# Kernel optimization log

Hardware: AMD Instinct MI355X
Metric: run time of the kernel (lower is better)

Reference implementation:

```python
import jax, jax.numpy as jnp
import numpy as np

N_NODES = 50000
N_EDGES = 600000
F_IN = 128
HID = 128
N_CLASSES = 10
N_GRAPHS = 64


def _glorot(key, shape):
    fan_in, fan_out = shape[1], shape[0]
    lim = float(np.sqrt(6.0 / (fan_in + fan_out)))
    return jax.random.uniform(key, shape, jnp.float32, -lim, lim)


def setup_inputs() -> dict:
    key = jax.random.key(0)
    ks = jax.random.split(key, 16)
    x = jax.random.normal(ks[0], (N_NODES, F_IN), jnp.float32)
    edge_index = jax.random.randint(ks[1], (2, N_EDGES), 0, N_NODES, jnp.int64)
    batch = jnp.sort(jax.random.randint(ks[2], (N_NODES,), 0, N_GRAPHS, jnp.int64))
    # GraphConv params: lin_rel (with bias) applied to aggregated neighbor sum,
    # lin_root (no bias) applied to the node's own features.
    params = dict(
        W1_rel=_glorot(ks[3], (HID, F_IN)), b1_rel=jnp.zeros((HID,), jnp.float32),
        W1_root=_glorot(ks[4], (HID, F_IN)),
        W2_rel=_glorot(ks[5], (HID, HID)), b2_rel=jnp.zeros((HID,), jnp.float32),
        W2_root=_glorot(ks[6], (HID, HID)),
        W3_rel=_glorot(ks[7], (HID, HID)), b3_rel=jnp.zeros((HID,), jnp.float32),
        W3_root=_glorot(ks[8], (HID, HID)),
        W_lin=_glorot(ks[9], (N_CLASSES, HID)), b_lin=jnp.zeros((N_CLASSES,), jnp.float32),
    )
    return {"x": x, "edge_index": edge_index, "batch": batch, **params}


def _graph_conv(x, src, dst, W_rel, b_rel, W_root):
    # gather source features, scatter-add into targets, then linear (sum aggr
    # commutes with the linear, matching PyG GraphConv which applies lin_rel
    # after aggregation)
    agg = jax.ops.segment_sum(x[src], dst, num_segments=N_NODES)  # [N, F]
    return agg @ W_rel.T + b_rel + x @ W_root.T


def _mean_pool(x, batch):
    sums = jax.ops.segment_sum(x, batch, num_segments=N_GRAPHS)  # [G, H]
    cnts = jax.ops.segment_sum(jnp.ones((x.shape[0],), x.dtype), batch,
                               num_segments=N_GRAPHS)
    return sums / jnp.maximum(cnts, 1.0)[:, None]


def reference(x, edge_index, batch,
              W1_rel, b1_rel, W1_root,
              W2_rel, b2_rel, W2_root,
              W3_rel, b3_rel, W3_root,
              W_lin, b_lin):
    src, dst = edge_index[0], edge_index[1]
    h = jax.nn.relu(_graph_conv(x, src, dst, W1_rel, b1_rel, W1_root))
    h = jax.nn.relu(_graph_conv(h, src, dst, W2_rel, b2_rel, W2_root))
    h = _graph_conv(h, src, dst, W3_rel, b3_rel, W3_root)
    g = _mean_pool(h, batch)  # [G, H]
    # dropout is identity in eval mode (training=False)
    return g @ W_lin.T + b_lin  # [G, num_classes]
```

## Files before the change

### kernel.cpp

```cpp
#include <hip/hip_runtime.h>
#include <hip/hip_bf16.h>

#define N_NODES   50000
#define N_EDGES   600000
#define F         128
#define N_GRAPHS  64
#define N_CLASSES 10
#define NPAD      50048
#define NB_SCAN   196
#define XCVT_BLOCKS 6250

typedef __attribute__((ext_vector_type(8))) short bf16x8;
typedef __attribute__((ext_vector_type(4))) float f32x4;

static __device__ __forceinline__ unsigned short f2bf(float f) {
    __hip_bfloat16 h = __float2bfloat16(f);
    return *reinterpret_cast<unsigned short*>(&h);
}
static __device__ __forceinline__ float bf2f(unsigned short u) {
    return __uint_as_float(((unsigned)u) << 16);
}

__global__ __launch_bounds__(256) void hist_kernel(
    const int* __restrict__ dst, int* __restrict__ deg)
{
    int e = blockIdx.x * 256 + threadIdx.x;
    if (e >= N_EDGES) return;
    atomicAdd(&deg[dst[e]], 1);
}

__global__ __launch_bounds__(256) void scanA_kernel(
    const int* __restrict__ deg, int* __restrict__ locEx, int* __restrict__ blockSum)
{
    __shared__ int sh[256];
    int t = threadIdx.x;
    int idx = blockIdx.x * 256 + t;
    int v = (idx < N_NODES) ? deg[idx] : 0;
    sh[t] = v;
    __syncthreads();
#pragma unroll
    for (int d = 1; d < 256; d <<= 1) {
        int u = (t >= d) ? sh[t - d] : 0;
        __syncthreads();
        sh[t] += u;
        __syncthreads();
    }
    if (idx < N_NODES) locEx[idx] = sh[t] - v;
    if (t == 255) blockSum[blockIdx.x] = sh[255];
}

__global__ __launch_bounds__(256) void scanBC_kernel(
    const int* __restrict__ locEx, const int* __restrict__ blockSum,
    int* __restrict__ off)
{
    __shared__ int sh[256];
    int t = threadIdx.x;
    int v = (t < NB_SCAN) ? blockSum[t] : 0;
    sh[t] = v;
    __syncthreads();
#pragma unroll
    for (int d = 1; d < 256; d <<= 1) {
        int u = (t >= d) ? sh[t - d] : 0;
        __syncthreads();
        sh[t] += u;
        __syncthreads();
    }
    int myVal  = blockSum[blockIdx.x];
    int base   = sh[blockIdx.x] - myVal;
    int idx = blockIdx.x * 256 + t;
    if (idx < N_NODES) off[idx] = locEx[idx] + base;
    if (blockIdx.x == 0 && t == 0) off[N_NODES] = sh[NB_SCAN - 1];
}

__global__ __launch_bounds__(256) void fill_kernel(
    const int* __restrict__ src, const int* __restrict__ dst,
    const int* __restrict__ off, int* __restrict__ cursor,
    int* __restrict__ csr_src)
{
    int e = blockIdx.x * 256 + threadIdx.x;
    if (e >= N_EDGES) return;
    int d = dst[e];
    int slot = atomicAdd(&cursor[d], 1);
    csr_src[off[d] + slot] = src[e];
}

__global__ __launch_bounds__(256) void cvt_all_kernel(
    const float* __restrict__ x,
    const float* __restrict__ W0, const float* __restrict__ W1,
    const float* __restrict__ W2, const float* __restrict__ W3,
    const float* __restrict__ W4, const float* __restrict__ W5,
    unsigned short* __restrict__ Xb, unsigned short* __restrict__ Wb)
{
    int b = blockIdx.x;
    if (b < XCVT_BLOCKS) {
        int i = b * 256 + threadIdx.x;
        float4 v = reinterpret_cast<const float4*>(x)[i];
        ushort4 o;
        o.x = f2bf(v.x); o.y = f2bf(v.y); o.z = f2bf(v.z); o.w = f2bf(v.w);
        reinterpret_cast<ushort4*>(Xb)[i] = o;
    } else {
        const int PER = (F * F / 4) / 256;
        int bb  = b - XCVT_BLOCKS;
        int mat = bb / PER;
        int i   = (bb % PER) * 256 + threadIdx.x;
        const float* W = (mat == 0) ? W0 : (mat == 1) ? W1 : (mat == 2) ? W2
                       : (mat == 3) ? W3 : (mat == 4) ? W4 : W5;
        float4 v = reinterpret_cast<const float4*>(W)[i];
        ushort4 o;
        o.x = f2bf(v.x); o.y = f2bf(v.y); o.z = f2bf(v.z); o.w = f2bf(v.w);
        reinterpret_cast<ushort4*>(Wb + (size_t)mat * F * F)[i] = o;
    }
}

template <int RELU>
__global__ __launch_bounds__(256) void conv_fused(
    const unsigned short* __restrict__ Xb,
    const int* __restrict__ off, const int* __restrict__ csr_src,
    const unsigned short* __restrict__ Wrel, const unsigned short* __restrict__ Wroot,
    const float* __restrict__ brel, unsigned short* __restrict__ H)
{
    __shared__ char AsRaw[64 * 256];
    const int t = threadIdx.x;
    const int mBase = blockIdx.x * 64;

    {
        const int r = t >> 2;
        const int q = t & 3;
        int row = mBase + r;
        float acc[32];
#pragma unroll
        for (int i = 0; i < 32; ++i) acc[i] = 0.f;
        if (row < N_NODES) {
            int s0 = off[row], s1 = off[row + 1];
            for (int j = s0; j < s1; ++j) {
                int s = csr_src[j];
                const bf16x8* base = reinterpret_cast<const bf16x8*>(
                    Xb + (size_t)s * F + q * 32);
#pragma unroll
                for (int c = 0; c < 4; ++c) {
                    bf16x8 v = base[c];
#pragma unroll
                    for (int e = 0; e < 8; ++e) acc[c * 8 + e] += bf2f((unsigned short)v[e]);
                }
            }
        }
#pragma unroll
        for (int c = 0; c < 4; ++c) {
            bf16x8 o;
#pragma unroll
            for (int e = 0; e < 8; ++e) o[e] = (short)f2bf(acc[c * 8 + e]);
            int bytecol = (q * 64 + c * 16) ^ ((r & 7) << 4);
            *reinterpret_cast<bf16x8*>(AsRaw + r * 256 + bytecol) = o;
        }
    }
    __syncthreads();

    const int wave = t >> 6;
    const int lane = t & 63;
    const int wm = wave >> 1, wn = wave & 1;
    const int m0l = wm * 32;
    const int n0  = wn * 64;
    const int lrow = lane & 15;
    const int lk8  = (lane >> 4) << 3;

    f32x4 acc[2][4];
#pragma unroll
    for (int mi = 0; mi < 2; ++mi)
#pragma unroll
        for (int ni = 0; ni < 4; ++ni)
            acc[mi][ni] = (f32x4){0.f, 0.f, 0.f, 0.f};

#pragma unroll
    for (int p = 0; p < 2; ++p) {
        const unsigned short* W = p ? Wroot : Wrel;
#pragma unroll
        for (int ks = 0; ks < 4; ++ks) {
            int k0 = ks * 32 + lk8;
            bf16x8 a[2], b[4];
#pragma unroll
            for (int mi = 0; mi < 2; ++mi) {
                int rl = m0l + mi * 16 + lrow;
                if (p == 0) {
                    int bytecol = (k0 * 2) ^ ((rl & 7) << 4);
                    a[mi] = *reinterpret_cast<const bf16x8*>(AsRaw + rl * 256 + bytecol);
                } else {
                    a[mi] = *reinterpret_cast<const bf16x8*>(
                        Xb + (size_t)(mBase + rl) * F + k0);
                }
            }
#pragma unroll
            for (int ni = 0; ni < 4; ++ni)
                b[ni] = *reinterpret_cast<const bf16x8*>(
                    W + (size_t)(n0 + ni * 16 + lrow) * F + k0);
#pragma unroll
            for (int mi = 0; mi < 2; ++mi)
#pragma unroll
                for (int ni = 0; ni < 4; ++ni)
                    acc[mi][ni] = __builtin_amdgcn_mfma_f32_16x16x32_bf16(
                        a[mi], b[ni], acc[mi][ni], 0, 0, 0);
        }
    }

    const int r0 = (lane >> 4) << 2;
#pragma unroll
    for (int ni = 0; ni < 4; ++ni) {
        int col = n0 + ni * 16 + lrow;
        float bb = brel[col];
#pragma unroll
        for (int mi = 0; mi < 2; ++mi) {
#pragma unroll
            for (int r = 0; r < 4; ++r) {
                int row = mBase + m0l + mi * 16 + r0 + r;
                if (row < N_NODES) {
                    float v = acc[mi][ni][r] + bb;
                    if (RELU) v = fmaxf(v, 0.f);
                    H[(size_t)row * F + col] = f2bf(v);
                }
            }
        }
    }
}

__global__ __launch_bounds__(256) void pool_kernel(
    const unsigned short* __restrict__ H, const int* __restrict__ batch,
    float* __restrict__ G)
{
    int g = blockIdx.x;
    int lo = 0, hi = N_NODES;
    while (lo < hi) { int m = (lo + hi) >> 1; if (batch[m] < g) lo = m + 1; else hi = m; }
    int start = lo;
    hi = N_NODES;
    while (lo < hi) { int m = (lo + hi) >> 1; if (batch[m] < g + 1) lo = m + 1; else hi = m; }
    int end = lo;

    int l8 = (threadIdx.x & 15) << 3;
    int rg = threadIdx.x >> 4;
    float acc[8] = {0.f, 0.f, 0.f, 0.f, 0.f, 0.f, 0.f, 0.f};
    for (int i = start + rg; i < end; i += 16) {
        bf16x8 v = *reinterpret_cast<const bf16x8*>(H + (size_t)i * F + l8);
#pragma unroll
        for (int r = 0; r < 8; ++r) acc[r] += bf2f((unsigned short)v[r]);
    }
    __shared__ float sh[16][F];
#pragma unroll
    for (int r = 0; r < 8; ++r) sh[rg][l8 + r] = acc[r];
    __syncthreads();
    if (threadIdx.x < F) {
        int f = threadIdx.x;
        float s = 0.f;
#pragma unroll
        for (int k = 0; k < 16; ++k) s += sh[k][f];
        float cnt = (float)(end - start);
        G[g * F + f] = s / fmaxf(cnt, 1.f);
    }
}

__global__ __launch_bounds__(640) void head_kernel(
    const float* __restrict__ G, const float* __restrict__ Wl,
    const float* __restrict__ bl, float* __restrict__ out)
{
    int t = threadIdx.x;
    int g = t / N_CLASSES;
    int c = t % N_CLASSES;
    float s = bl[c];
#pragma unroll 8
    for (int k = 0; k < F; ++k) s += G[g * F + k] * Wl[c * F + k];
    out[t] = s;
}

extern "C" void kernel_launch(void* const* d_in, const int* in_sizes, int n_in,
                              void* d_out, int out_size, void* d_ws, size_t ws_size,
                              hipStream_t stream)
{
    const float* x     = (const float*)d_in[0];
    const int*   edge  = (const int*)d_in[1];
    const int*   src   = edge;
    const int*   dst   = edge + N_EDGES;
    const int*   batch = (const int*)d_in[2];
    const float* W1r = (const float*)d_in[3];
    const float* b1  = (const float*)d_in[4];
    const float* W1o = (const float*)d_in[5];
    const float* W2r = (const float*)d_in[6];
    const float* b2  = (const float*)d_in[7];
    const float* W2o = (const float*)d_in[8];
    const float* W3r = (const float*)d_in[9];
    const float* b3  = (const float*)d_in[10];
    const float* W3o = (const float*)d_in[11];
    const float* Wl  = (const float*)d_in[12];
    const float* bl  = (const float*)d_in[13];
    float* out = (float*)d_out;

    char* ws = (char*)d_ws;
    const size_t fb = (size_t)NPAD * F * sizeof(unsigned short);
    unsigned short* Xb  = (unsigned short*)ws;
    unsigned short* H1b = (unsigned short*)(ws + fb);
    unsigned short* H2b = (unsigned short*)(ws + 2 * fb);
    char* p = ws + 3 * fb;
    unsigned short* Wb = (unsigned short*)p;
    p += (size_t)6 * F * F * sizeof(unsigned short);
    float* G = (float*)p;                p += (size_t)N_GRAPHS * F * sizeof(float);
    int* deg     = (int*)p;              p += (size_t)N_NODES * sizeof(int);
    int* cursor  = (int*)p;              p += (size_t)N_NODES * sizeof(int);
    int* off     = (int*)p;              p += (size_t)(N_NODES + 1) * sizeof(int);
    int* locEx   = (int*)p;              p += (size_t)N_NODES * sizeof(int);
    int* blockSum= (int*)p;              p += (size_t)256 * sizeof(int);
    int* csr_src = (int*)p;

    const int edgeBlocks = (N_EDGES + 255) / 256;
    const int convBlocks = NPAD / 64;
    const int cvtBlocks  = XCVT_BLOCKS + 6 * (F * F / 4) / 256;

    cvt_all_kernel<<<cvtBlocks, 256, 0, stream>>>(x, W1r, W1o, W2r, W2o, W3r, W3o, Xb, Wb);

    hipMemsetAsync(deg, 0, (size_t)2 * N_NODES * sizeof(int), stream);
    hist_kernel<<<edgeBlocks, 256, 0, stream>>>(dst, deg);
    scanA_kernel<<<NB_SCAN, 256, 0, stream>>>(deg, locEx, blockSum);
    scanBC_kernel<<<NB_SCAN, 256, 0, stream>>>(locEx, blockSum, off);
    fill_kernel<<<edgeBlocks, 256, 0, stream>>>(src, dst, off, cursor, csr_src);

    conv_fused<1><<<convBlocks, 256, 0, stream>>>(Xb,  off, csr_src, Wb + 0 * F * F, Wb + 1 * F * F, b1, H1b);
    conv_fused<1><<<convBlocks, 256, 0, stream>>>(H1b, off, csr_src, Wb + 2 * F * F, Wb + 3 * F * F, b2, H2b);
    conv_fused<0><<<convBlocks, 256, 0, stream>>>(H2b, off, csr_src, Wb + 4 * F * F, Wb + 5 * F * F, b3, H1b);

    pool_kernel<<<N_GRAPHS, 256, 0, stream>>>(H1b, batch, G);
    head_kernel<<<1, 640, 0, stream>>>(G, Wl, bl, out);
}
```

Baseline: 253.2 us.

## Halve conv tile rows, spread gather over 8 lanes per node, prefetch neighbor

Each conv block now handles 32 nodes instead of 64. Each node's neighbor aggregation is split across 8 threads of 16 features instead of 4 threads of 32. The gather loop software-prefetches the next neighbor's row before accumulating the current one. The aim is more gather parallelism and more blocks in flight to hide the latency of irregular memory accesses, at the cost of loading the weight tiles twice as often per node and doing half the MFMA work per wave.

Result: slower. 290.3 us (+14.7%).

```diff
diff --git a/kernel.cpp b/kernel.cpp
--- a/kernel.cpp
+++ b/kernel.cpp
@@ -9,6 +9,7 @@
 #define NPAD      50048
 #define NB_SCAN   196
 #define XCVT_BLOCKS 6250
+#define BM        32
 
 typedef __attribute__((ext_vector_type(8))) short bf16x8;
 typedef __attribute__((ext_vector_type(4))) float f32x4;
@@ -119,56 +120,66 @@
     const unsigned short* __restrict__ Wrel, const unsigned short* __restrict__ Wroot,
     const float* __restrict__ brel, unsigned short* __restrict__ H)
 {
-    __shared__ char AsRaw[64 * 256];
+    __shared__ char AsRaw[BM * 256];
     const int t = threadIdx.x;
-    const int mBase = blockIdx.x * 64;
+    const int mBase = blockIdx.x * BM;
 
     {
-        const int r = t >> 2;
-        const int q = t & 3;
+        const int r = t >> 3;
+        const int q = t & 7;
         int row = mBase + r;
-        float acc[32];
-#pragma unroll
-        for (int i = 0; i < 32; ++i) acc[i] = 0.f;
+        float acc[16];
+#pragma unroll
+        for (int i = 0; i < 16; ++i) acc[i] = 0.f;
         if (row < N_NODES) {
             int s0 = off[row], s1 = off[row + 1];
-            for (int j = s0; j < s1; ++j) {
-                int s = csr_src[j];
-                const bf16x8* base = reinterpret_cast<const bf16x8*>(
-                    Xb + (size_t)s * F + q * 32);
-#pragma unroll
-                for (int c = 0; c < 4; ++c) {
-                    bf16x8 v = base[c];
-#pragma unroll
-                    for (int e = 0; e < 8; ++e) acc[c * 8 + e] += bf2f((unsigned short)v[e]);
+            const unsigned short* Xq = Xb + (size_t)q * 16;
+            if (s0 < s1) {
+                int s = csr_src[s0];
+                bf16x8 v0 = *reinterpret_cast<const bf16x8*>(Xq + (size_t)s * F);
+                bf16x8 v1 = *reinterpret_cast<const bf16x8*>(Xq + (size_t)s * F + 8);
+                for (int j = s0 + 1; j < s1; ++j) {
+                    int sn = csr_src[j];
+                    bf16x8 u0 = *reinterpret_cast<const bf16x8*>(Xq + (size_t)sn * F);
+                    bf16x8 u1 = *reinterpret_cast<const bf16x8*>(Xq + (size_t)sn * F + 8);
+#pragma unroll
+                    for (int e = 0; e < 8; ++e) {
+                        acc[e]     += bf2f((unsigned short)v0[e]);
+                        acc[8 + e] += bf2f((unsigned short)v1[e]);
+                    }
+                    v0 = u0; v1 = u1;
+                }
+#pragma unroll
+                for (int e = 0; e < 8; ++e) {
+                    acc[e]     += bf2f((unsigned short)v0[e]);
+                    acc[8 + e] += bf2f((unsigned short)v1[e]);
                 }
             }
         }
-#pragma unroll
-        for (int c = 0; c < 4; ++c) {
-            bf16x8 o;
-#pragma unroll
-            for (int e = 0; e < 8; ++e) o[e] = (short)f2bf(acc[c * 8 + e]);
-            int bytecol = (q * 64 + c * 16) ^ ((r & 7) << 4);
-            *reinterpret_cast<bf16x8*>(AsRaw + r * 256 + bytecol) = o;
+        bf16x8 o0, o1;
+#pragma unroll
+        for (int e = 0; e < 8; ++e) {
+            o0[e] = (short)f2bf(acc[e]);
+            o1[e] = (short)f2bf(acc[8 + e]);
         }
+        int sw = (r & 7) << 4;
+        *reinterpret_cast<bf16x8*>(AsRaw + r * 256 + ((q * 32)      ^ sw)) = o0;
+        *reinterpret_cast<bf16x8*>(AsRaw + r * 256 + ((q * 32 + 16) ^ sw)) = o1;
     }
     __syncthreads();
 
     const int wave = t >> 6;
     const int lane = t & 63;
     const int wm = wave >> 1, wn = wave & 1;
-    const int m0l = wm * 32;
+    const int m0l = wm * 16;
     const int n0  = wn * 64;
     const int lrow = lane & 15;
     const int lk8  = (lane >> 4) << 3;
-
-    f32x4 acc[2][4];
-#pragma unroll
-    for (int mi = 0; mi < 2; ++mi)
-#pragma unroll
-        for (int ni = 0; ni < 4; ++ni)
-            acc[mi][ni] = (f32x4){0.f, 0.f, 0.f, 0.f};
+    const int arow = m0l + lrow;
+
+    f32x4 acc2[4];
+#pragma unroll
+    for (int ni = 0; ni < 4; ++ni) acc2[ni] = (f32x4){0.f, 0.f, 0.f, 0.f};
 
 #pragma unroll
     for (int p = 0; p < 2; ++p) {
@@ -176,28 +187,22 @@
 #pragma unroll
         for (int ks = 0; ks < 4; ++ks) {
             int k0 = ks * 32 + lk8;
-            bf16x8 a[2], b[4];
-#pragma unroll
-            for (int mi = 0; mi < 2; ++mi) {
-                int rl = m0l + mi * 16 + lrow;
-                if (p == 0) {
-                    int bytecol = (k0 * 2) ^ ((rl & 7) << 4);
-                    a[mi] = *reinterpret_cast<const bf16x8*>(AsRaw + rl * 256 + bytecol);
-                } else {
-                    a[mi] = *reinterpret_cast<const bf16x8*>(
-                        Xb + (size_t)(mBase + rl) * F + k0);
-                }
+            bf16x8 a, b[4];
+            if (p == 0) {
+                int bytecol = (k0 * 2) ^ ((arow & 7) << 4);
+                a = *reinterpret_cast<const bf16x8*>(AsRaw + arow * 256 + bytecol);
+            } else {
+                a = *reinterpret_cast<const bf16x8*>(
+                    Xb + (size_t)(mBase + arow) * F + k0);
             }
 #pragma unroll
             for (int ni = 0; ni < 4; ++ni)
                 b[ni] = *reinterpret_cast<const bf16x8*>(
                     W + (size_t)(n0 + ni * 16 + lrow) * F + k0);
 #pragma unroll
-            for (int mi = 0; mi < 2; ++mi)
-#pragma unroll
-                for (int ni = 0; ni < 4; ++ni)
-                    acc[mi][ni] = __builtin_amdgcn_mfma_f32_16x16x32_bf16(
-                        a[mi], b[ni], acc[mi][ni], 0, 0, 0);
+            for (int ni = 0; ni < 4; ++ni)
+                acc2[ni] = __builtin_amdgcn_mfma_f32_16x16x32_bf16(
+                    a, b[ni], acc2[ni], 0, 0, 0);
         }
     }
 
@@ -207,15 +212,12 @@
         int col = n0 + ni * 16 + lrow;
         float bb = brel[col];
 #pragma unroll
-        for (int mi = 0; mi < 2; ++mi) {
-#pragma unroll
-            for (int r = 0; r < 4; ++r) {
-                int row = mBase + m0l + mi * 16 + r0 + r;
-                if (row < N_NODES) {
-                    float v = acc[mi][ni][r] + bb;
-                    if (RELU) v = fmaxf(v, 0.f);
-                    H[(size_t)row * F + col] = f2bf(v);
-                }
+        for (int r = 0; r < 4; ++r) {
+            int row = mBase + m0l + r0 + r;
+            if (row < N_NODES) {
+                float v = acc2[ni][r] + bb;
+                if (RELU) v = fmaxf(v, 0.f);
+                H[(size_t)row * F + col] = f2bf(v);
             }
         }
     }
@@ -307,7 +309,7 @@
     int* csr_src = (int*)p;
 
     const int edgeBlocks = (N_EDGES + 255) / 256;
-    const int convBlocks = NPAD / 64;
+    const int convBlocks = NPAD / BM;
     const int cvtBlocks  = XCVT_BLOCKS + 6 * (F * F / 4) / 256;
 
     cvt_all_kernel<<<cvtBlocks, 256, 0, stream>>>(x, W1r, W1o, W2r, W2o, W3r, W3o, Xb, Wb);
```

## Slice features into XCD-local planes and split gather from MFMA conv

Applied to the files above, without the earlier changes.

Stores node features as four 32-column planes (64 bytes per node per plane) instead of row-major 256-byte rows. Each conv layer is split into a separate gather kernel and an MFMA GEMM kernel. The gather kernel maps blocks so each XCD handles a single feature plane, so each plane's working set (~3.2MB) can stay in that XCD's L2 during random neighbor gathers, and it prefetches the next neighbor row. The cost is an extra round trip of the aggregated tensor through global memory and twice as many kernel launches per layer.

New measurement: 266.2 us. 5.1% more time.

```diff
diff --git a/kernel.cpp b/kernel.cpp
--- a/kernel.cpp
+++ b/kernel.cpp
@@ -9,6 +9,7 @@
 #define NPAD      50048
 #define NB_SCAN   196
 #define XCVT_BLOCKS 6250
+#define PE        ((size_t)NPAD * 32)
 
 typedef __attribute__((ext_vector_type(8))) short bf16x8;
 typedef __attribute__((ext_vector_type(4))) float f32x4;
@@ -89,15 +90,17 @@
     const float* __restrict__ W0, const float* __restrict__ W1,
     const float* __restrict__ W2, const float* __restrict__ W3,
     const float* __restrict__ W4, const float* __restrict__ W5,
-    unsigned short* __restrict__ Xb, unsigned short* __restrict__ Wb)
+    unsigned short* __restrict__ Xs, unsigned short* __restrict__ Wb)
 {
     int b = blockIdx.x;
     if (b < XCVT_BLOCKS) {
         int i = b * 256 + threadIdx.x;
+        int n  = i >> 5;
+        int f4 = (i & 31) << 2;
         float4 v = reinterpret_cast<const float4*>(x)[i];
         ushort4 o;
         o.x = f2bf(v.x); o.y = f2bf(v.y); o.z = f2bf(v.z); o.w = f2bf(v.w);
-        reinterpret_cast<ushort4*>(Xb)[i] = o;
+        *reinterpret_cast<ushort4*>(Xs + (size_t)(f4 >> 5) * PE + (size_t)n * 32 + (f4 & 31)) = o;
     } else {
         const int PER = (F * F / 4) / 256;
         int bb  = b - XCVT_BLOCKS;
@@ -112,54 +115,55 @@
     }
 }
 
+__global__ __launch_bounds__(256) void gather_sliced(
+    const unsigned short* __restrict__ Xs, const int* __restrict__ off,
+    const int* __restrict__ csr_src, unsigned short* __restrict__ AGGs)
+{
+    const int b    = blockIdx.x;
+    const int xcd  = b & 7;
+    const int s    = xcd & 3;
+    const int tile = ((b >> 3) << 1) | (xcd >> 2);
+    const int r    = threadIdx.x >> 2;
+    const int fq   = threadIdx.x & 3;
+    const int row  = tile * 64 + r;
+
+    const unsigned short* Xp = Xs + (size_t)s * PE + fq * 8;
+    float acc[8] = {0.f, 0.f, 0.f, 0.f, 0.f, 0.f, 0.f, 0.f};
+
+    if (row < N_NODES) {
+        int j0 = off[row], j1 = off[row + 1];
+        if (j0 < j1) {
+            int sc = csr_src[j0];
+            bf16x8 v = *reinterpret_cast<const bf16x8*>(Xp + (size_t)sc * 32);
+            for (int j = j0 + 1; j < j1; ++j) {
+                int sn = csr_src[j];
+                bf16x8 u = *reinterpret_cast<const bf16x8*>(Xp + (size_t)sn * 32);
+#pragma unroll
+                for (int e = 0; e < 8; ++e) acc[e] += bf2f((unsigned short)v[e]);
+                v = u;
+            }
+#pragma unroll
+            for (int e = 0; e < 8; ++e) acc[e] += bf2f((unsigned short)v[e]);
+        }
+    }
+    bf16x8 o;
+#pragma unroll
+    for (int e = 0; e < 8; ++e) o[e] = (short)f2bf(acc[e]);
+    *reinterpret_cast<bf16x8*>(AGGs + (size_t)s * PE + (size_t)row * 32 + fq * 8) = o;
+}
+
 template <int RELU>
-__global__ __launch_bounds__(256) void conv_fused(
-    const unsigned short* __restrict__ Xb,
-    const int* __restrict__ off, const int* __restrict__ csr_src,
+__global__ __launch_bounds__(256) void conv_mfma(
+    const unsigned short* __restrict__ AGGs, const unsigned short* __restrict__ Xs,
     const unsigned short* __restrict__ Wrel, const unsigned short* __restrict__ Wroot,
-    const float* __restrict__ brel, unsigned short* __restrict__ H)
-{
-    __shared__ char AsRaw[64 * 256];
-    const int t = threadIdx.x;
-    const int mBase = blockIdx.x * 64;
-
-    {
-        const int r = t >> 2;
-        const int q = t & 3;
-        int row = mBase + r;
-        float acc[32];
-#pragma unroll
-        for (int i = 0; i < 32; ++i) acc[i] = 0.f;
-        if (row < N_NODES) {
-            int s0 = off[row], s1 = off[row + 1];
-            for (int j = s0; j < s1; ++j) {
-                int s = csr_src[j];
-                const bf16x8* base = reinterpret_cast<const bf16x8*>(
-                    Xb + (size_t)s * F + q * 32);
-#pragma unroll
-                for (int c = 0; c < 4; ++c) {
-                    bf16x8 v = base[c];
-#pragma unroll
-                    for (int e = 0; e < 8; ++e) acc[c * 8 + e] += bf2f((unsigned short)v[e]);
-                }
-            }
-        }
-#pragma unroll
-        for (int c = 0; c < 4; ++c) {
-            bf16x8 o;
-#pragma unroll
-            for (int e = 0; e < 8; ++e) o[e] = (short)f2bf(acc[c * 8 + e]);
-            int bytecol = (q * 64 + c * 16) ^ ((r & 7) << 4);
-            *reinterpret_cast<bf16x8*>(AsRaw + r * 256 + bytecol) = o;
-        }
-    }
-    __syncthreads();
-
+    const float* __restrict__ brel, unsigned short* __restrict__ Hs)
+{
+    const int t    = threadIdx.x;
     const int wave = t >> 6;
     const int lane = t & 63;
     const int wm = wave >> 1, wn = wave & 1;
-    const int m0l = wm * 32;
-    const int n0  = wn * 64;
+    const int m0 = blockIdx.x * 64 + wm * 32;
+    const int n0 = wn * 64;
     const int lrow = lane & 15;
     const int lk8  = (lane >> 4) << 3;
 
@@ -172,26 +176,19 @@
 
 #pragma unroll
     for (int p = 0; p < 2; ++p) {
+        const unsigned short* A = p ? Xs : AGGs;
         const unsigned short* W = p ? Wroot : Wrel;
 #pragma unroll
         for (int ks = 0; ks < 4; ++ks) {
-            int k0 = ks * 32 + lk8;
             bf16x8 a[2], b[4];
 #pragma unroll
-            for (int mi = 0; mi < 2; ++mi) {
-                int rl = m0l + mi * 16 + lrow;
-                if (p == 0) {
-                    int bytecol = (k0 * 2) ^ ((rl & 7) << 4);
-                    a[mi] = *reinterpret_cast<const bf16x8*>(AsRaw + rl * 256 + bytecol);
-                } else {
-                    a[mi] = *reinterpret_cast<const bf16x8*>(
-                        Xb + (size_t)(mBase + rl) * F + k0);
-                }
-            }
+            for (int mi = 0; mi < 2; ++mi)
+                a[mi] = *reinterpret_cast<const bf16x8*>(
+                    A + (size_t)ks * PE + (size_t)(m0 + mi * 16 + lrow) * 32 + lk8);
 #pragma unroll
             for (int ni = 0; ni < 4; ++ni)
                 b[ni] = *reinterpret_cast<const bf16x8*>(
-                    W + (size_t)(n0 + ni * 16 + lrow) * F + k0);
+                    W + (size_t)(n0 + ni * 16 + lrow) * F + ks * 32 + lk8);
 #pragma unroll
             for (int mi = 0; mi < 2; ++mi)
 #pragma unroll
@@ -206,15 +203,16 @@
     for (int ni = 0; ni < 4; ++ni) {
         int col = n0 + ni * 16 + lrow;
         float bb = brel[col];
+        size_t cplane = (size_t)(col >> 5) * PE + (col & 31);
 #pragma unroll
         for (int mi = 0; mi < 2; ++mi) {
 #pragma unroll
             for (int r = 0; r < 4; ++r) {
-                int row = mBase + m0l + mi * 16 + r0 + r;
+                int row = m0 + mi * 16 + r0 + r;
                 if (row < N_NODES) {
                     float v = acc[mi][ni][r] + bb;
                     if (RELU) v = fmaxf(v, 0.f);
-                    H[(size_t)row * F + col] = f2bf(v);
+                    Hs[cplane + (size_t)row * 32] = f2bf(v);
                 }
             }
         }
@@ -222,7 +220,7 @@
 }
 
 __global__ __launch_bounds__(256) void pool_kernel(
-    const unsigned short* __restrict__ H, const int* __restrict__ batch,
+    const unsigned short* __restrict__ Hs, const int* __restrict__ batch,
     float* __restrict__ G)
 {
     int g = blockIdx.x;
@@ -235,9 +233,10 @@
 
     int l8 = (threadIdx.x & 15) << 3;
     int rg = threadIdx.x >> 4;
+    const unsigned short* Hp = Hs + (size_t)(l8 >> 5) * PE + (l8 & 31);
     float acc[8] = {0.f, 0.f, 0.f, 0.f, 0.f, 0.f, 0.f, 0.f};
     for (int i = start + rg; i < end; i += 16) {
-        bf16x8 v = *reinterpret_cast<const bf16x8*>(H + (size_t)i * F + l8);
+        bf16x8 v = *reinterpret_cast<const bf16x8*>(Hp + (size_t)i * 32);
 #pragma unroll
         for (int r = 0; r < 8; ++r) acc[r] += bf2f((unsigned short)v[r]);
     }
@@ -292,10 +291,11 @@
 
     char* ws = (char*)d_ws;
     const size_t fb = (size_t)NPAD * F * sizeof(unsigned short);
-    unsigned short* Xb  = (unsigned short*)ws;
-    unsigned short* H1b = (unsigned short*)(ws + fb);
-    unsigned short* H2b = (unsigned short*)(ws + 2 * fb);
-    char* p = ws + 3 * fb;
+    unsigned short* Xs   = (unsigned short*)ws;
+    unsigned short* AGGs = (unsigned short*)(ws + fb);
+    unsigned short* H1s  = (unsigned short*)(ws + 2 * fb);
+    unsigned short* H2s  = (unsigned short*)(ws + 3 * fb);
+    char* p = ws + 4 * fb;
     unsigned short* Wb = (unsigned short*)p;
     p += (size_t)6 * F * F * sizeof(unsigned short);
     float* G = (float*)p;                p += (size_t)N_GRAPHS * F * sizeof(float);
@@ -306,11 +306,12 @@
     int* blockSum= (int*)p;              p += (size_t)256 * sizeof(int);
     int* csr_src = (int*)p;
 
-    const int edgeBlocks = (N_EDGES + 255) / 256;
-    const int convBlocks = NPAD / 64;
-    const int cvtBlocks  = XCVT_BLOCKS + 6 * (F * F / 4) / 256;
-
-    cvt_all_kernel<<<cvtBlocks, 256, 0, stream>>>(x, W1r, W1o, W2r, W2o, W3r, W3o, Xb, Wb);
+    const int edgeBlocks   = (N_EDGES + 255) / 256;
+    const int convBlocks   = NPAD / 64;
+    const int gatherBlocks = (NPAD / 64 / 2) * 8;
+    const int cvtBlocks    = XCVT_BLOCKS + 6 * (F * F / 4) / 256;
+
+    cvt_all_kernel<<<cvtBlocks, 256, 0, stream>>>(x, W1r, W1o, W2r, W2o, W3r, W3o, Xs, Wb);
 
     hipMemsetAsync(deg, 0, (size_t)2 * N_NODES * sizeof(int), stream);
     hist_kernel<<<edgeBlocks, 256, 0, stream>>>(dst, deg);
@@ -318,10 +319,13 @@
     scanBC_kernel<<<NB_SCAN, 256, 0, stream>>>(locEx, blockSum, off);
     fill_kernel<<<edgeBlocks, 256, 0, stream>>>(src, dst, off, cursor, csr_src);
 
-    conv_fused<1><<<convBlocks, 256, 0, stream>>>(Xb,  off, csr_src, Wb + 0 * F * F, Wb + 1 * F * F, b1, H1b);
-    conv_fused<1><<<convBlocks, 256, 0, stream>>>(H1b, off, csr_src, Wb + 2 * F * F, Wb + 3 * F * F, b2, H2b);
-    conv_fused<0><<<convBlocks, 256, 0, stream>>>(H2b, off, csr_src, Wb + 4 * F * F, Wb + 5 * F * F, b3, H1b);
-
-    pool_kernel<<<N_GRAPHS, 256, 0, stream>>>(H1b, batch, G);
+    gather_sliced<<<gatherBlocks, 256, 0, stream>>>(Xs,  off, csr_src, AGGs);
+    conv_mfma<1><<<convBlocks, 256, 0, stream>>>(AGGs, Xs,  Wb + 0 * F * F, Wb + 1 * F * F, b1, H1s);
+    gather_sliced<<<gatherBlocks, 256, 0, stream>>>(H1s, off, csr_src, AGGs);
+    conv_mfma<1><<<convBlocks, 256, 0, stream>>>(AGGs, H1s, Wb + 2 * F * F, Wb + 3 * F * F, b2, H2s);
+    gather_sliced<<<gatherBlocks, 256, 0, stream>>>(H2s, off, csr_src, AGGs);
+    conv_mfma<0><<<convBlocks, 256, 0, stream>>>(AGGs, H2s, Wb + 4 * F * F, Wb + 5 * F * F, b3, H1s);
+
+    pool_kernel<<<N_GRAPHS, 256, 0, stream>>>(H1s, batch, G);
     head_kernel<<<1, 640, 0, stream>>>(G, Wl, bl, out);
 }
```

## Sort CSR neighbor lists and gather in source-range chunks with block syncs

Applied to the files above, without the earlier changes.

Adds a per-node insertion sort so each CSR neighbor list is in ascending source order. The gather loop in the fused conv kernel then walks the source ID space in eight chunks, with a __syncthreads between chunks, so threads in a block touch similar regions of the feature matrix at the same time. The aim is better L2/cache locality for the random neighbor gathers. The cost is an extra sort kernel, eight block barriers per conv block, and extra branching, which can serialize warps that have uneven degrees.

New measurement: 351.3 us. 1.39x slower.

```diff
diff --git a/kernel.cpp b/kernel.cpp
--- a/kernel.cpp
+++ b/kernel.cpp
@@ -9,6 +9,7 @@
 #define NPAD      50048
 #define NB_SCAN   196
 #define XCVT_BLOCKS 6250
+#define NCHUNK    8
 
 typedef __attribute__((ext_vector_type(8))) short bf16x8;
 typedef __attribute__((ext_vector_type(4))) float f32x4;
@@ -82,6 +83,20 @@
     int d = dst[e];
     int slot = atomicAdd(&cursor[d], 1);
     csr_src[off[d] + slot] = src[e];
+}
+
+__global__ __launch_bounds__(256) void sort_kernel(
+    const int* __restrict__ off, int* __restrict__ csr_src)
+{
+    int n = blockIdx.x * 256 + threadIdx.x;
+    if (n >= N_NODES) return;
+    int s0 = off[n], s1 = off[n + 1];
+    for (int i = s0 + 1; i < s1; ++i) {
+        int v = csr_src[i];
+        int j = i - 1;
+        while (j >= s0 && csr_src[j] > v) { csr_src[j + 1] = csr_src[j]; --j; }
+        csr_src[j + 1] = v;
+    }
 }
 
 __global__ __launch_bounds__(256) void cvt_all_kernel(
@@ -130,26 +145,31 @@
         float acc[32];
 #pragma unroll
         for (int i = 0; i < 32; ++i) acc[i] = 0.f;
-        if (row < N_NODES) {
-            int s0 = off[row], s1 = off[row + 1];
-            for (int j = s0; j < s1; ++j) {
+        int j = 0, s1 = 0;
+        if (row < N_NODES) { j = off[row]; s1 = off[row + 1]; }
+        const unsigned short* Xq = Xb + (size_t)q * 32;
+        for (int c = 1; c <= NCHUNK; ++c) {
+            int bound = (c == NCHUNK) ? N_NODES : c * (N_NODES / NCHUNK);
+            while (j < s1) {
                 int s = csr_src[j];
-                const bf16x8* base = reinterpret_cast<const bf16x8*>(
-                    Xb + (size_t)s * F + q * 32);
-#pragma unroll
-                for (int c = 0; c < 4; ++c) {
-                    bf16x8 v = base[c];
-#pragma unroll
-                    for (int e = 0; e < 8; ++e) acc[c * 8 + e] += bf2f((unsigned short)v[e]);
+                if (s >= bound) break;
+                const bf16x8* base = reinterpret_cast<const bf16x8*>(Xq + (size_t)s * F);
+#pragma unroll
+                for (int cc = 0; cc < 4; ++cc) {
+                    bf16x8 v = base[cc];
+#pragma unroll
+                    for (int e = 0; e < 8; ++e) acc[cc * 8 + e] += bf2f((unsigned short)v[e]);
                 }
+                ++j;
             }
+            __syncthreads();
         }
 #pragma unroll
-        for (int c = 0; c < 4; ++c) {
+        for (int cc = 0; cc < 4; ++cc) {
             bf16x8 o;
 #pragma unroll
-            for (int e = 0; e < 8; ++e) o[e] = (short)f2bf(acc[c * 8 + e]);
-            int bytecol = (q * 64 + c * 16) ^ ((r & 7) << 4);
+            for (int e = 0; e < 8; ++e) o[e] = (short)f2bf(acc[cc * 8 + e]);
+            int bytecol = (q * 64 + cc * 16) ^ ((r & 7) << 4);
             *reinterpret_cast<bf16x8*>(AsRaw + r * 256 + bytecol) = o;
         }
     }
@@ -317,6 +337,7 @@
     scanA_kernel<<<NB_SCAN, 256, 0, stream>>>(deg, locEx, blockSum);
     scanBC_kernel<<<NB_SCAN, 256, 0, stream>>>(locEx, blockSum, off);
     fill_kernel<<<edgeBlocks, 256, 0, stream>>>(src, dst, off, cursor, csr_src);
+    sort_kernel<<<NB_SCAN, 256, 0, stream>>>(off, csr_src);
 
     conv_fused<1><<<convBlocks, 256, 0, stream>>>(Xb,  off, csr_src, Wb + 0 * F * F, Wb + 1 * F * F, b1, H1b);
     conv_fused<1><<<convBlocks, 256, 0, stream>>>(H1b, off, csr_src, Wb + 2 * F * F, Wb + 3 * F * F, b2, H2b);
```
